# Kernel tuning notes

Hardware: AMD Instinct MI355X
Metric: run time of the kernel (lower is better)

## Reference

```python
import jax, jax.numpy as jnp
import numpy as np

N = 20000
E = 640000
F_IN = 128
HID = 64
HEADS = 4
OUT = 10
NUM_GRAPHS = 128
NEG_SLOPE = 0.2
BN_EPS = 1e-5


def setup_inputs() -> dict:
    key = jax.random.key(0)
    ks = jax.random.split(key, 24)
    x = jax.random.normal(ks[0], (N, F_IN), dtype=jnp.float32)
    edge_index = jax.random.randint(ks[1], (2, E), 0, N, dtype=jnp.int32)
    batch = jnp.sort(jax.random.randint(ks[2], (N,), 0, NUM_GRAPHS, dtype=jnp.int32))
    s = 0.05
    HC = HEADS * HID  # 256
    inp = {
        'x': x, 'edge_index': edge_index, 'batch': batch,
        # GATConv 1: in=128 -> heads*64, concat
        'W1': jax.random.normal(ks[3], (F_IN, HC)) * s,
        'as1': jax.random.normal(ks[4], (HEADS, HID)) * s,
        'ad1': jax.random.normal(ks[5], (HEADS, HID)) * s,
        'b1': jnp.zeros((HC,), jnp.float32),
        'g1': jnp.ones((HC,), jnp.float32),
        'be1': jnp.zeros((HC,), jnp.float32),
        # GATConv 2: in=256 -> heads*64, concat
        'W2': jax.random.normal(ks[6], (HC, HC)) * s,
        'as2': jax.random.normal(ks[7], (HEADS, HID)) * s,
        'ad2': jax.random.normal(ks[8], (HEADS, HID)) * s,
        'b2': jnp.zeros((HC,), jnp.float32),
        'g2': jnp.ones((HC,), jnp.float32),
        'be2': jnp.zeros((HC,), jnp.float32),
        # GATConv 3: in=256 -> 64, concat=False (mean over heads)
        'W3': jax.random.normal(ks[9], (HC, HC)) * s,
        'as3': jax.random.normal(ks[10], (HEADS, HID)) * s,
        'ad3': jax.random.normal(ks[11], (HEADS, HID)) * s,
        'b3': jnp.zeros((HID,), jnp.float32),
        # final Linear 64 -> 10
        'Wlin': jax.random.normal(ks[12], (HID, OUT)) * s,
        'blin': jnp.zeros((OUT,), jnp.float32),
    }
    return inp


def _gat_conv(x, src, dst, W, a_src, a_dst, b, concat):
    # PyG GATConv: h = x @ W -> [N,H,C]; alpha_e = leaky_relu(as[src]+ad[dst]);
    # softmax over edges grouped by destination; scatter-add alpha*h[src].
    h = (x @ W).reshape(N, HEADS, HID)
    a_s = jnp.einsum('nhc,hc->nh', h, a_src)  # [N,H]
    a_d = jnp.einsum('nhc,hc->nh', h, a_dst)
    e = jax.nn.leaky_relu(a_s[src] + a_d[dst], NEG_SLOPE)  # [E,H]
    m = jax.ops.segment_max(e, dst, num_segments=N)  # per-dst max, stable softmax
    e = jnp.exp(e - m[dst])
    denom = jax.ops.segment_sum(e, dst, num_segments=N)
    alpha = e / (denom[dst] + 1e-16)  # [E,H]
    out = jax.ops.segment_sum(h[src] * alpha[:, :, None], dst, num_segments=N)  # [N,H,C]
    if concat:
        out = out.reshape(N, HEADS * HID)
    else:
        out = out.mean(axis=1)
    return out + b


def _bn(x, g, b):
    # BatchNorm1d (training-mode batch statistics)
    mu = x.mean(0)
    var = x.var(0)
    return (x - mu) * jax.lax.rsqrt(var + BN_EPS) * g + b


def reference(x, edge_index, batch, W1, as1, ad1, b1, g1, be1,
              W2, as2, ad2, b2, g2, be2, W3, as3, ad3, b3, Wlin, blin):
    # add self-loops (PyG GATConv default add_self_loops=True)
    loops = jnp.arange(N, dtype=edge_index.dtype)
    src = jnp.concatenate([edge_index[0], loops])
    dst = jnp.concatenate([edge_index[1], loops])

    xs = []
    h = _gat_conv(x, src, dst, W1, as1, ad1, b1, concat=True)
    h = _bn(h, g1, be1)
    xs.append(h)
    h = jax.nn.elu(h)  # dropout is identity in eval mode

    h = _gat_conv(h, src, dst, W2, as2, ad2, b2, concat=True)
    h = _bn(h, g2, be2)
    xs.append(h)
    h = jax.nn.elu(h)

    h = _gat_conv(h, src, dst, W3, as3, ad3, b3, concat=False)
    xs.append(h)

    # global_mean_pool over graphs
    sums = jax.ops.segment_sum(h, batch, num_segments=NUM_GRAPHS)
    cnt = jax.ops.segment_sum(jnp.ones((N,), h.dtype), batch, num_segments=NUM_GRAPHS)
    pooled = sums / jnp.maximum(cnt, 1.0)[:, None]
    xs.append(pooled)

    out = pooled @ Wlin + blin
    return (out, *xs)
```

## Files before the change

### kernel.cpp

```cpp
#include <hip/hip_runtime.h>
#include <hip/hip_bf16.h>
#include <math.h>

#define N_NODES 20000
#define N_EDGES 640000
#define F_IN 128
#define HID 64
#define HEADS 4
#define HC 256
#define OUT_DIM 10
#define NUM_GRAPHS 128
#define NEG_SLOPE 0.2f
#define BN_EPS 1e-5f
#define CONV_N (N_NODES * F_IN / 4)
#define ELL_CAP 128

typedef short bf16s;
typedef unsigned short u16;
using bf16x8 = __attribute__((ext_vector_type(8))) short;
using bf16x4 = __attribute__((ext_vector_type(4))) short;
using f32x4 = __attribute__((ext_vector_type(4))) float;

__device__ __forceinline__ float bs2f(short s) {
    unsigned int u = ((unsigned int)(unsigned short)s) << 16;
    return __builtin_bit_cast(float, u);
}
__device__ __forceinline__ short f2bs(float f) {
    unsigned int u = __builtin_bit_cast(unsigned int, f);
    unsigned int r = u + 0x7FFFu + ((u >> 16) & 1u);
    return (short)(r >> 16);
}


__global__ void prep_all(const float* __restrict__ x, bf16s* __restrict__ xb,
                         const float* __restrict__ W1, const float* __restrict__ W2,
                         const float* __restrict__ W3,
                         bf16s* __restrict__ Wt1, bf16s* __restrict__ Wt2,
                         bf16s* __restrict__ Wt3,
                         int* __restrict__ cnt, u16* __restrict__ ell,
                         float* __restrict__ colstats, int* __restrict__ counter) {
    int tid = blockIdx.x * blockDim.x + threadIdx.x;
    if (tid < CONV_N) {
        float4 v = reinterpret_cast<const float4*>(x)[tid];
        bf16x4 o;
        o[0] = f2bs(v.x); o[1] = f2bs(v.y); o[2] = f2bs(v.z); o[3] = f2bs(v.w);
        reinterpret_cast<bf16x4*>(xb)[tid] = o;
        return;
    }
    tid -= CONV_N;
    if (tid < HC * F_IN) { int c = tid >> 7, k = tid & 127; Wt1[tid] = f2bs(W1[(size_t)k * HC + c]); return; }
    tid -= HC * F_IN;
    if (tid < HC * HC) { int c = tid >> 8, k = tid & 255; Wt2[tid] = f2bs(W2[(size_t)k * HC + c]); return; }
    tid -= HC * HC;
    if (tid < HC * HC) { int c = tid >> 8, k = tid & 255; Wt3[tid] = f2bs(W3[(size_t)k * HC + c]); return; }
    tid -= HC * HC;
    if (tid < N_NODES) {
        cnt[tid] = 1;
        ell[(size_t)tid * ELL_CAP] = (u16)tid;
        return;
    }
    tid -= N_NODES;
    if (tid < 2 * HC) { colstats[tid] = 0.f; return; }
    tid -= 2 * HC;
    if (tid == 0) *counter = 0;
}


__global__ void fill_ell(const int* __restrict__ ei, int* cnt, u16* __restrict__ ell, int E) {
    int tid = blockIdx.x * blockDim.x + threadIdx.x;
    if (tid < E) {
        int src = ei[tid];
        int dst = ei[E + tid];
        int pos = atomicAdd(&cnt[dst], 1);
        if (pos < ELL_CAP) ell[(size_t)dst * ELL_CAP + pos] = (u16)src;
    }
}


__global__ __launch_bounds__(256) void gemm_bf16(
        const bf16s* __restrict__ A, const bf16s* __restrict__ Wt,
        bf16s* __restrict__ Hout,
        const float* __restrict__ a_src, const float* __restrict__ a_dst,
        float* __restrict__ asb, float* __restrict__ adb,
        int M, int K) {
    __shared__ bf16s As[128][72];
    __shared__ bf16s Bs[128][72];
    int tid = threadIdx.x;
    int wave = tid >> 6, lane = tid & 63;
    int row0 = blockIdx.x * 128;
    int head2 = blockIdx.y;
    int col0 = head2 * 128;
    int lr = lane & 15, lk = lane >> 4;

    f32x4 acc[2][8];
    #pragma unroll
    for (int i = 0; i < 2; i++)
        #pragma unroll
        for (int j = 0; j < 8; j++)
            acc[i][j] = (f32x4){0.f, 0.f, 0.f, 0.f};

    for (int k0 = 0; k0 < K; k0 += 64) {
        #pragma unroll
        for (int i = 0; i < 4; i++) {
            int idx = tid + i * 256;
            int r = idx >> 3, ch = idx & 7;
            int gr = row0 + r;
            bf16x8 v = {};
            if (gr < M) v = *reinterpret_cast<const bf16x8*>(A + (size_t)gr * K + k0 + ch * 8);
            *reinterpret_cast<bf16x8*>(&As[r][ch * 8]) = v;
        }
        #pragma unroll
        for (int i = 0; i < 4; i++) {
            int idx = tid + i * 256;
            int r = idx >> 3, ch = idx & 7;
            bf16x8 v = *reinterpret_cast<const bf16x8*>(Wt + (size_t)(col0 + r) * K + k0 + ch * 8);
            *reinterpret_cast<bf16x8*>(&Bs[r][ch * 8]) = v;
        }
        __syncthreads();
        #pragma unroll
        for (int ks = 0; ks < 2; ks++) {
            bf16x8 bfr[8];
            #pragma unroll
            for (int j = 0; j < 8; j++)
                bfr[j] = *reinterpret_cast<const bf16x8*>(&Bs[j * 16 + lr][ks * 32 + lk * 8]);
            #pragma unroll
            for (int i = 0; i < 2; i++) {
                bf16x8 afr = *reinterpret_cast<const bf16x8*>(&As[wave * 32 + i * 16 + lr][ks * 32 + lk * 8]);
                #pragma unroll
                for (int j = 0; j < 8; j++)
                    acc[i][j] = __builtin_amdgcn_mfma_f32_16x16x32_bf16(afr, bfr[j], acc[i][j], 0, 0, 0);
            }
        }
        __syncthreads();
    }

    #pragma unroll
    for (int i = 0; i < 2; i++) {
        #pragma unroll
        for (int q = 0; q < 4; q++) {
            int r = row0 + wave * 32 + i * 16 + lk * 4 + q;
            if (r < M) {
                #pragma unroll
                for (int j = 0; j < 8; j++) {
                    int c = col0 + j * 16 + lr;
                    Hout[(size_t)r * HC + c] = f2bs(acc[i][j][q]);
                }
            }
        }
    }

    float asv[8], adv[8];
    #pragma unroll
    for (int j = 0; j < 8; j++) {
        asv[j] = a_src[col0 + j * 16 + lr];
        adv[j] = a_dst[col0 + j * 16 + lr];
    }
    #pragma unroll
    for (int i = 0; i < 2; i++) {
        #pragma unroll
        for (int q = 0; q < 4; q++) {
            float ps0 = acc[i][0][q] * asv[0] + acc[i][1][q] * asv[1] + acc[i][2][q] * asv[2] + acc[i][3][q] * asv[3];
            float pd0 = acc[i][0][q] * adv[0] + acc[i][1][q] * adv[1] + acc[i][2][q] * adv[2] + acc[i][3][q] * adv[3];
            float ps1 = acc[i][4][q] * asv[4] + acc[i][5][q] * asv[5] + acc[i][6][q] * asv[6] + acc[i][7][q] * asv[7];
            float pd1 = acc[i][4][q] * adv[4] + acc[i][5][q] * adv[5] + acc[i][6][q] * adv[6] + acc[i][7][q] * adv[7];
            #pragma unroll
            for (int off = 1; off < 16; off <<= 1) {
                ps0 += __shfl_xor(ps0, off);
                pd0 += __shfl_xor(pd0, off);
                ps1 += __shfl_xor(ps1, off);
                pd1 += __shfl_xor(pd1, off);
            }
            int r = row0 + wave * 32 + i * 16 + lk * 4 + q;
            if (lr == 0 && r < M) {
                asb[r * HEADS + head2 * 2 + 0] = ps0;
                adb[r * HEADS + head2 * 2 + 0] = pd0;
                asb[r * HEADS + head2 * 2 + 1] = ps1;
                adb[r * HEADS + head2 * 2 + 1] = pd1;
            }
        }
    }
}


__device__ __forceinline__ float lrelu(float x) { return x > 0.f ? x : NEG_SLOPE * x; }

template<int MODE>
__global__ __launch_bounds__(256) void gat_aggregate(
        const bf16s* __restrict__ hfeat,
        const float* __restrict__ asb, const float* __restrict__ adb,
        const int* __restrict__ cnt, const u16* __restrict__ ell,
        const float* __restrict__ bias,
        float* __restrict__ out) {
    __shared__ float4 exps[4][ELL_CAP];
    __shared__ int    srcs[4][ELL_CAP];
    int wid = threadIdx.x >> 6, lane = threadIdx.x & 63;
    int d = blockIdx.x * 4 + wid;
    int deg = min(cnt[d], ELL_CAP);
    const u16* row = ell + (size_t)d * ELL_CAP;

    float adv0 = adb[d * HEADS + 0], adv1 = adb[d * HEADS + 1];
    float adv2 = adb[d * HEADS + 2], adv3 = adb[d * HEADS + 3];

    float s0 = 0.f, s1 = 0.f, s2 = 0.f, s3 = 0.f;
    for (int j = lane; j < deg; j += 64) {
        int s = row[j];
        const float4 av = *reinterpret_cast<const float4*>(asb + (size_t)s * HEADS);
        float e0 = __expf(lrelu(av.x + adv0));
        float e1 = __expf(lrelu(av.y + adv1));
        float e2 = __expf(lrelu(av.z + adv2));
        float e3 = __expf(lrelu(av.w + adv3));
        float4 ev; ev.x = e0; ev.y = e1; ev.z = e2; ev.w = e3;
        exps[wid][j] = ev;
        srcs[wid][j] = s;
        s0 += e0; s1 += e1; s2 += e2; s3 += e3;
    }
    #pragma unroll
    for (int off = 32; off > 0; off >>= 1) {
        s0 += __shfl_xor(s0, off);
        s1 += __shfl_xor(s1, off);
        s2 += __shfl_xor(s2, off);
        s3 += __shfl_xor(s3, off);
    }
    float r0 = 1.f / (s0 + 1e-16f), r1 = 1.f / (s1 + 1e-16f);
    float r2 = 1.f / (s2 + 1e-16f), r3 = 1.f / (s3 + 1e-16f);

    int half = lane >> 5;
    int cl = lane & 31;
    int hsel = cl >> 3;
    float rdh = (hsel == 0) ? r0 : (hsel == 1) ? r1 : (hsel == 2) ? r2 : r3;
    const float* expf_base = reinterpret_cast<const float*>(&exps[wid][0]);

    float a0 = 0.f, a1 = 0.f, a2 = 0.f, a3 = 0.f, a4 = 0.f, a5 = 0.f, a6 = 0.f, a7 = 0.f;
    float b0 = 0.f, b1 = 0.f, b2 = 0.f, b3 = 0.f, b4 = 0.f, b5 = 0.f, b6 = 0.f, b7 = 0.f;

    int nfull = deg & ~3;
    for (int j = 0; j < nfull; j += 4) {
        int iA = j + half;
        int iB = j + 2 + half;
        int sA = srcs[wid][iA];
        int sB = srcs[wid][iB];
        float alA = expf_base[iA * 4 + hsel] * rdh;
        float alB = expf_base[iB * 4 + hsel] * rdh;
        const bf16x8 vA = *reinterpret_cast<const bf16x8*>(hfeat + (size_t)sA * HC + cl * 8);
        const bf16x8 vB = *reinterpret_cast<const bf16x8*>(hfeat + (size_t)sB * HC + cl * 8);
        a0 += alA * bs2f(vA[0]); a1 += alA * bs2f(vA[1]);
        a2 += alA * bs2f(vA[2]); a3 += alA * bs2f(vA[3]);
        a4 += alA * bs2f(vA[4]); a5 += alA * bs2f(vA[5]);
        a6 += alA * bs2f(vA[6]); a7 += alA * bs2f(vA[7]);
        b0 += alB * bs2f(vB[0]); b1 += alB * bs2f(vB[1]);
        b2 += alB * bs2f(vB[2]); b3 += alB * bs2f(vB[3]);
        b4 += alB * bs2f(vB[4]); b5 += alB * bs2f(vB[5]);
        b6 += alB * bs2f(vB[6]); b7 += alB * bs2f(vB[7]);
    }
    for (int j = nfull + half; j < deg; j += 2) {
        int s = srcs[wid][j];
        float al = expf_base[j * 4 + hsel] * rdh;
        const bf16x8 v = *reinterpret_cast<const bf16x8*>(hfeat + (size_t)s * HC + cl * 8);
        a0 += al * bs2f(v[0]); a1 += al * bs2f(v[1]);
        a2 += al * bs2f(v[2]); a3 += al * bs2f(v[3]);
        a4 += al * bs2f(v[4]); a5 += al * bs2f(v[5]);
        a6 += al * bs2f(v[6]); a7 += al * bs2f(v[7]);
    }
    float av0 = a0 + b0, av1 = a1 + b1, av2 = a2 + b2, av3 = a3 + b3;
    float av4 = a4 + b4, av5 = a5 + b5, av6 = a6 + b6, av7 = a7 + b7;

    av0 += __shfl_xor(av0, 32); av1 += __shfl_xor(av1, 32);
    av2 += __shfl_xor(av2, 32); av3 += __shfl_xor(av3, 32);
    av4 += __shfl_xor(av4, 32); av5 += __shfl_xor(av5, 32);
    av6 += __shfl_xor(av6, 32); av7 += __shfl_xor(av7, 32);

    if constexpr (MODE == 0) {
        if (half == 0) {
            const float4 bb0 = *reinterpret_cast<const float4*>(bias + cl * 8);
            const float4 bb1 = *reinterpret_cast<const float4*>(bias + cl * 8 + 4);
            av0 += bb0.x; av1 += bb0.y; av2 += bb0.z; av3 += bb0.w;
            av4 += bb1.x; av5 += bb1.y; av6 += bb1.z; av7 += bb1.w;
            float4 o0; o0.x = av0; o0.y = av1; o0.z = av2; o0.w = av3;
            float4 o1; o1.x = av4; o1.y = av5; o1.z = av6; o1.w = av7;
            *reinterpret_cast<float4*>(out + (size_t)d * HC + cl * 8) = o0;
            *reinterpret_cast<float4*>(out + (size_t)d * HC + cl * 8 + 4) = o1;
        }
    } else {
        float h0 = av0 + __shfl_xor(av0, 8); h0 += __shfl_xor(h0, 16);
        float h1 = av1 + __shfl_xor(av1, 8); h1 += __shfl_xor(h1, 16);
        float h2 = av2 + __shfl_xor(av2, 8); h2 += __shfl_xor(h2, 16);
        float h3 = av3 + __shfl_xor(av3, 8); h3 += __shfl_xor(h3, 16);
        float h4 = av4 + __shfl_xor(av4, 8); h4 += __shfl_xor(h4, 16);
        float h5 = av5 + __shfl_xor(av5, 8); h5 += __shfl_xor(h5, 16);
        float h6 = av6 + __shfl_xor(av6, 8); h6 += __shfl_xor(h6, 16);
        float h7 = av7 + __shfl_xor(av7, 8); h7 += __shfl_xor(h7, 16);
        if (half == 0 && cl < 8) {
            int c = cl * 8;
            float4 o0, o1;
            o0.x = 0.25f * h0 + bias[c + 0]; o0.y = 0.25f * h1 + bias[c + 1];
            o0.z = 0.25f * h2 + bias[c + 2]; o0.w = 0.25f * h3 + bias[c + 3];
            o1.x = 0.25f * h4 + bias[c + 4]; o1.y = 0.25f * h5 + bias[c + 5];
            o1.z = 0.25f * h6 + bias[c + 6]; o1.w = 0.25f * h7 + bias[c + 7];
            *reinterpret_cast<float4*>(out + (size_t)d * HID + c) = o0;
            *reinterpret_cast<float4*>(out + (size_t)d * HID + c + 4) = o1;
        }
    }
}


__global__ void bn_stats_fin(const float* __restrict__ x, float* colsum, float* colsq,
                             const float* __restrict__ g, const float* __restrict__ be,
                             float* scale, float* shift, int* counter, int n) {
    __shared__ int lastFlag;
    int col = threadIdx.x;
    float s = 0.f, q = 0.f;
    for (int r = blockIdx.x; r < n; r += gridDim.x) {
        float v = x[(size_t)r * HC + col];
        s += v;
        q += v * v;
    }
    atomicAdd(&colsum[col], s);
    atomicAdd(&colsq[col], q);
    __syncthreads();
    if (threadIdx.x == 0) {
        __threadfence();
        int prev = atomicAdd(counter, 1);
        lastFlag = (prev == (int)gridDim.x - 1) ? 1 : 0;
    }
    __syncthreads();
    if (lastFlag) {
        __threadfence();
        float cs = ((volatile float*)colsum)[col];
        float cq = ((volatile float*)colsq)[col];
        float mu = cs / (float)n;
        float var = cq / (float)n - mu * mu;
        float sc = g[col] * rsqrtf(var + BN_EPS);
        scale[col] = sc;
        shift[col] = be[col] - mu * sc;
        colsum[col] = 0.f;
        colsq[col] = 0.f;
        if (threadIdx.x == 0) *counter = 0;
    }
}

__global__ void bn_apply_elu(const float* __restrict__ x,
                             const float* __restrict__ scale, const float* __restrict__ shift,
                             float* __restrict__ xs_out, bf16s* __restrict__ act, int n) {
    int col = threadIdx.x;
    float sc = scale[col], sh = shift[col];
    for (int r = blockIdx.x; r < n; r += gridDim.x) {
        float v = x[(size_t)r * HC + col];
        float y = v * sc + sh;
        xs_out[(size_t)r * HC + col] = y;
        float e = y > 0.f ? y : __expf(y) - 1.f;
        act[(size_t)r * HC + col] = f2bs(e);
    }
}


__global__ __launch_bounds__(256) void pool_final(
        const float* __restrict__ xs2, const int* __restrict__ batch,
        const float* __restrict__ Wlin, const float* __restrict__ blin,
        float* __restrict__ pooled_out, float* __restrict__ out_final) {
    __shared__ float red[4][HID];
    int g = blockIdx.x;
    int tid = threadIdx.x;
    int w = tid >> 6, lane = tid & 63;

    int lo = 0, hi = N_NODES;
    while (lo < hi) { int mid = (lo + hi) >> 1; if (batch[mid] < g) lo = mid + 1; else hi = mid; }
    int a = lo;
    lo = 0; hi = N_NODES;
    while (lo < hi) { int mid = (lo + hi) >> 1; if (batch[mid] < g + 1) lo = mid + 1; else hi = mid; }
    int b = lo;

    float acc = 0.f;
    for (int n = a + w; n < b; n += 4) acc += xs2[(size_t)n * HID + lane];
    red[w][lane] = acc;
    __syncthreads();

    if (w == 0) {
        float pooled = (red[0][lane] + red[1][lane] + red[2][lane] + red[3][lane])
                       / fmaxf((float)(b - a), 1.f);
        pooled_out[g * HID + lane] = pooled;
        #pragma unroll
        for (int o = 0; o < OUT_DIM; o++) {
            float p = pooled * Wlin[lane * OUT_DIM + o];
            #pragma unroll
            for (int off = 32; off > 0; off >>= 1) p += __shfl_xor(p, off);
            if (lane == 0) out_final[g * OUT_DIM + o] = p + blin[o];
        }
    }
}


extern "C" void kernel_launch(void* const* d_in, const int* in_sizes, int n_in,
                              void* d_out, int out_size, void* d_ws, size_t ws_size,
                              hipStream_t stream) {
    const float* x     = (const float*)d_in[0];
    const int*   ei    = (const int*)d_in[1];
    const int*   batch = (const int*)d_in[2];
    const float* W1  = (const float*)d_in[3];
    const float* as1 = (const float*)d_in[4];
    const float* ad1 = (const float*)d_in[5];
    const float* b1  = (const float*)d_in[6];
    const float* g1  = (const float*)d_in[7];
    const float* be1 = (const float*)d_in[8];
    const float* W2  = (const float*)d_in[9];
    const float* as2 = (const float*)d_in[10];
    const float* ad2 = (const float*)d_in[11];
    const float* b2  = (const float*)d_in[12];
    const float* g2  = (const float*)d_in[13];
    const float* be2 = (const float*)d_in[14];
    const float* W3  = (const float*)d_in[15];
    const float* as3 = (const float*)d_in[16];
    const float* ad3 = (const float*)d_in[17];
    const float* b3  = (const float*)d_in[18];
    const float* Wlin = (const float*)d_in[19];
    const float* blin = (const float*)d_in[20];

    float* out_final = (float*)d_out;
    float* xs0 = out_final + NUM_GRAPHS * OUT_DIM;
    float* xs1 = xs0 + (size_t)N_NODES * HC;
    float* xs2 = xs1 + (size_t)N_NODES * HC;
    float* pooled_out = xs2 + (size_t)N_NODES * HID;

    char* p = (char*)d_ws;
    auto alloc = [&](size_t bytes) { char* r = p; p += (bytes + 255) & ~(size_t)255; return (void*)r; };
    bf16s* hfeat  = (bf16s*)alloc((size_t)N_NODES * HC * 2);
    bf16s* actC   = (bf16s*)alloc((size_t)N_NODES * HC * 2);
    bf16s* xb     = (bf16s*)alloc((size_t)N_NODES * F_IN * 2);
    float* gatB   = (float*)alloc((size_t)N_NODES * HC * 4);
    bf16s* Wt1    = (bf16s*)alloc((size_t)HC * F_IN * 2);
    bf16s* Wt2    = (bf16s*)alloc((size_t)HC * HC * 2);
    bf16s* Wt3    = (bf16s*)alloc((size_t)HC * HC * 2);
    float* asb    = (float*)alloc((size_t)N_NODES * HEADS * 4);
    float* adb    = (float*)alloc((size_t)N_NODES * HEADS * 4);
    int*   cnt    = (int*)alloc((size_t)N_NODES * 4);
    u16*   ell    = (u16*)alloc((size_t)N_NODES * ELL_CAP * 2);
    float* colstats = (float*)alloc(2 * HC * 4);
    float* colsum = colstats;
    float* colsq  = colstats + HC;
    float* scale  = (float*)alloc(HC * 4);
    float* shift  = (float*)alloc(HC * 4);
    int*   counter = (int*)alloc(256);

    const int PREP_TOT = CONV_N + HC * F_IN + 2 * HC * HC + N_NODES + 2 * HC + 1;

    prep_all<<<(PREP_TOT + 255) / 256, 256, 0, stream>>>(x, xb, W1, W2, W3, Wt1, Wt2, Wt3,
                                                         cnt, ell, colstats, counter);
    fill_ell<<<(N_EDGES + 255) / 256, 256, 0, stream>>>(ei, cnt, ell, N_EDGES);

    int agg_blocks = N_NODES / 4;
    dim3 ggrid((N_NODES + 127) / 128, HEADS / 2);

    {
        gemm_bf16<<<ggrid, 256, 0, stream>>>(xb, Wt1, hfeat, as1, ad1, asb, adb, N_NODES, F_IN);
        gat_aggregate<0><<<agg_blocks, 256, 0, stream>>>(hfeat, asb, adb, cnt, ell, b1, gatB);
        bn_stats_fin<<<512, 256, 0, stream>>>(gatB, colsum, colsq, g1, be1, scale, shift, counter, N_NODES);
        bn_apply_elu<<<2048, 256, 0, stream>>>(gatB, scale, shift, xs0, actC, N_NODES);
    }
    {
        gemm_bf16<<<ggrid, 256, 0, stream>>>(actC, Wt2, hfeat, as2, ad2, asb, adb, N_NODES, HC);
        gat_aggregate<0><<<agg_blocks, 256, 0, stream>>>(hfeat, asb, adb, cnt, ell, b2, gatB);
        bn_stats_fin<<<512, 256, 0, stream>>>(gatB, colsum, colsq, g2, be2, scale, shift, counter, N_NODES);
        bn_apply_elu<<<2048, 256, 0, stream>>>(gatB, scale, shift, xs1, actC, N_NODES);
    }
    {
        gemm_bf16<<<ggrid, 256, 0, stream>>>(actC, Wt3, hfeat, as3, ad3, asb, adb, N_NODES, HC);
        gat_aggregate<1><<<agg_blocks, 256, 0, stream>>>(hfeat, asb, adb, cnt, ell, b3, xs2);
    }
    pool_final<<<NUM_GRAPHS, 256, 0, stream>>>(xs2, batch, Wlin, blin, pooled_out, out_final);
}
```

Measured before the change: 296.0 us.

## Fuse softmax normalization into aggregation loop, dropping LDS staging pass

The GAT aggregate kernel no longer runs a first pass that computes per-edge exponentials and stores them with source indices in shared memory. Each lane now computes the exp for its own head inline while gathering features, accumulates an unnormalized sum and a running denominator, and divides once at the end. This removes a separate pass, the shared-memory traffic and one wave-wide reduction. In exchange each of the eight lanes covering a head recomputes the same exp and re-reads the index and attention score from global memory.

```diff
diff --git a/kernel.cpp b/kernel.cpp
--- a/kernel.cpp
+++ b/kernel.cpp
@@ -191,83 +191,59 @@
         const int* __restrict__ cnt, const u16* __restrict__ ell,
         const float* __restrict__ bias,
         float* __restrict__ out) {
-    __shared__ float4 exps[4][ELL_CAP];
-    __shared__ int    srcs[4][ELL_CAP];
     int wid = threadIdx.x >> 6, lane = threadIdx.x & 63;
     int d = blockIdx.x * 4 + wid;
     int deg = min(cnt[d], ELL_CAP);
     const u16* row = ell + (size_t)d * ELL_CAP;
 
-    float adv0 = adb[d * HEADS + 0], adv1 = adb[d * HEADS + 1];
-    float adv2 = adb[d * HEADS + 2], adv3 = adb[d * HEADS + 3];
-
-    float s0 = 0.f, s1 = 0.f, s2 = 0.f, s3 = 0.f;
-    for (int j = lane; j < deg; j += 64) {
-        int s = row[j];
-        const float4 av = *reinterpret_cast<const float4*>(asb + (size_t)s * HEADS);
-        float e0 = __expf(lrelu(av.x + adv0));
-        float e1 = __expf(lrelu(av.y + adv1));
-        float e2 = __expf(lrelu(av.z + adv2));
-        float e3 = __expf(lrelu(av.w + adv3));
-        float4 ev; ev.x = e0; ev.y = e1; ev.z = e2; ev.w = e3;
-        exps[wid][j] = ev;
-        srcs[wid][j] = s;
-        s0 += e0; s1 += e1; s2 += e2; s3 += e3;
-    }
-    #pragma unroll
-    for (int off = 32; off > 0; off >>= 1) {
-        s0 += __shfl_xor(s0, off);
-        s1 += __shfl_xor(s1, off);
-        s2 += __shfl_xor(s2, off);
-        s3 += __shfl_xor(s3, off);
-    }
-    float r0 = 1.f / (s0 + 1e-16f), r1 = 1.f / (s1 + 1e-16f);
-    float r2 = 1.f / (s2 + 1e-16f), r3 = 1.f / (s3 + 1e-16f);
-
     int half = lane >> 5;
     int cl = lane & 31;
     int hsel = cl >> 3;
-    float rdh = (hsel == 0) ? r0 : (hsel == 1) ? r1 : (hsel == 2) ? r2 : r3;
-    const float* expf_base = reinterpret_cast<const float*>(&exps[wid][0]);
-
+    float adh = adb[d * HEADS + hsel];
+
+    float sa = 0.f, sb = 0.f;
     float a0 = 0.f, a1 = 0.f, a2 = 0.f, a3 = 0.f, a4 = 0.f, a5 = 0.f, a6 = 0.f, a7 = 0.f;
     float b0 = 0.f, b1 = 0.f, b2 = 0.f, b3 = 0.f, b4 = 0.f, b5 = 0.f, b6 = 0.f, b7 = 0.f;
 
     int nfull = deg & ~3;
     for (int j = 0; j < nfull; j += 4) {
-        int iA = j + half;
-        int iB = j + 2 + half;
-        int sA = srcs[wid][iA];
-        int sB = srcs[wid][iB];
-        float alA = expf_base[iA * 4 + hsel] * rdh;
-        float alB = expf_base[iB * 4 + hsel] * rdh;
+        int sA = row[j + half];
+        int sB = row[j + 2 + half];
+        float eA = __expf(lrelu(asb[(size_t)sA * HEADS + hsel] + adh));
+        float eB = __expf(lrelu(asb[(size_t)sB * HEADS + hsel] + adh));
         const bf16x8 vA = *reinterpret_cast<const bf16x8*>(hfeat + (size_t)sA * HC + cl * 8);
         const bf16x8 vB = *reinterpret_cast<const bf16x8*>(hfeat + (size_t)sB * HC + cl * 8);
-        a0 += alA * bs2f(vA[0]); a1 += alA * bs2f(vA[1]);
-        a2 += alA * bs2f(vA[2]); a3 += alA * bs2f(vA[3]);
-        a4 += alA * bs2f(vA[4]); a5 += alA * bs2f(vA[5]);
-        a6 += alA * bs2f(vA[6]); a7 += alA * bs2f(vA[7]);
-        b0 += alB * bs2f(vB[0]); b1 += alB * bs2f(vB[1]);
-        b2 += alB * bs2f(vB[2]); b3 += alB * bs2f(vB[3]);
-        b4 += alB * bs2f(vB[4]); b5 += alB * bs2f(vB[5]);
-        b6 += alB * bs2f(vB[6]); b7 += alB * bs2f(vB[7]);
+        sa += eA; sb += eB;
+        a0 += eA * bs2f(vA[0]); a1 += eA * bs2f(vA[1]);
+        a2 += eA * bs2f(vA[2]); a3 += eA * bs2f(vA[3]);
+        a4 += eA * bs2f(vA[4]); a5 += eA * bs2f(vA[5]);
+        a6 += eA * bs2f(vA[6]); a7 += eA * bs2f(vA[7]);
+        b0 += eB * bs2f(vB[0]); b1 += eB * bs2f(vB[1]);
+        b2 += eB * bs2f(vB[2]); b3 += eB * bs2f(vB[3]);
+        b4 += eB * bs2f(vB[4]); b5 += eB * bs2f(vB[5]);
+        b6 += eB * bs2f(vB[6]); b7 += eB * bs2f(vB[7]);
     }
     for (int j = nfull + half; j < deg; j += 2) {
-        int s = srcs[wid][j];
-        float al = expf_base[j * 4 + hsel] * rdh;
+        int s = row[j];
+        float e = __expf(lrelu(asb[(size_t)s * HEADS + hsel] + adh));
         const bf16x8 v = *reinterpret_cast<const bf16x8*>(hfeat + (size_t)s * HC + cl * 8);
-        a0 += al * bs2f(v[0]); a1 += al * bs2f(v[1]);
-        a2 += al * bs2f(v[2]); a3 += al * bs2f(v[3]);
-        a4 += al * bs2f(v[4]); a5 += al * bs2f(v[5]);
-        a6 += al * bs2f(v[6]); a7 += al * bs2f(v[7]);
-    }
+        sa += e;
+        a0 += e * bs2f(v[0]); a1 += e * bs2f(v[1]);
+        a2 += e * bs2f(v[2]); a3 += e * bs2f(v[3]);
+        a4 += e * bs2f(v[4]); a5 += e * bs2f(v[5]);
+        a6 += e * bs2f(v[6]); a7 += e * bs2f(v[7]);
+    }
+    float ssum = sa + sb;
+    ssum += __shfl_xor(ssum, 32);
     float av0 = a0 + b0, av1 = a1 + b1, av2 = a2 + b2, av3 = a3 + b3;
     float av4 = a4 + b4, av5 = a5 + b5, av6 = a6 + b6, av7 = a7 + b7;
-
     av0 += __shfl_xor(av0, 32); av1 += __shfl_xor(av1, 32);
     av2 += __shfl_xor(av2, 32); av3 += __shfl_xor(av3, 32);
     av4 += __shfl_xor(av4, 32); av5 += __shfl_xor(av5, 32);
     av6 += __shfl_xor(av6, 32); av7 += __shfl_xor(av7, 32);
+    float rdh = 1.f / (ssum + 1e-16f);
+    av0 *= rdh; av1 *= rdh; av2 *= rdh; av3 *= rdh;
+    av4 *= rdh; av5 *= rdh; av6 *= rdh; av7 *= rdh;
 
     if constexpr (MODE == 0) {
         if (half == 0) {
```

Measured after the change: 309.2 us. 4.4% more time.
